# Optimization experiments

Measured on AMD Instinct MI355X. Metric: run time of the kernel, lower is better.

## Reference

```python
import jax, jax.numpy as jnp
import numpy as np


def setup_inputs() -> dict:
    key = jax.random.key(0)
    k1, k2 = jax.random.split(key)
    x = jax.random.normal(k1, (16, 512, 64, 64), dtype=jnp.float32)
    # learned scalar (nn.Parameter init zeros; use small random value so output is nontrivial)
    gamma = jax.random.normal(k2, (1,), dtype=jnp.float32) * 0.1
    return {"x": x, "gamma": gamma}


def reference(x, gamma):
    b, c, h, w = x.shape
    q = x.reshape(b, c, h * w)                      # [b, c, hw]
    energy = jnp.einsum('bcn,bdn->bcd', q, q)       # [b, c, c]
    # reverse-max trick: max - energy, then softmax over last dim
    energy_new = jnp.max(energy, axis=-1, keepdims=True) - energy
    attention = jax.nn.softmax(energy_new, axis=-1)  # [b, c, c]
    out = jnp.einsum('bcd,bdn->bcn', attention, q).reshape(b, c, h, w)
    return gamma * out + x
```

## Files before the change

### kernel.cpp

```cpp
#include <hip/hip_runtime.h>


constexpr int Bb = 16;
constexpr int Cc = 512;
constexpr int NN = 4096;

typedef _Float16 half8 __attribute__((ext_vector_type(8)));
typedef _Float16 half4 __attribute__((ext_vector_type(4)));
typedef float float4v __attribute__((ext_vector_type(4)));

__device__ inline void gld_lds16(const _Float16* g, _Float16* l) {
    __builtin_amdgcn_global_load_lds(
        (const __attribute__((address_space(1))) unsigned int*)g,
        (__attribute__((address_space(3))) unsigned int*)l, 16, 0, 0);
}

__global__ __launch_bounds__(256) void prep_kernel(const float* __restrict__ x,
                                                   _Float16* __restrict__ Qh,
                                                   _Float16* __restrict__ QhT) {
    __shared__ float T[64][65];
    const int b = blockIdx.z;
    const int n0 = blockIdx.x * 64;
    const int d0 = blockIdx.y * 64;
    const float* xb = x + ((size_t)b * Cc + d0) * NN + n0;
    const int tid = threadIdx.x;
#pragma unroll
    for (int i = 0; i < 4; ++i) {
        int lin = tid + i * 256;
        int dr = lin >> 4;
        int c4 = (lin & 15) * 4;
        float4 v = *reinterpret_cast<const float4*>(&xb[(size_t)dr * NN + c4]);
        T[dr][c4 + 0] = v.x; T[dr][c4 + 1] = v.y;
        T[dr][c4 + 2] = v.z; T[dr][c4 + 3] = v.w;
    }
    __syncthreads();
#pragma unroll
    for (int i = 0; i < 2; ++i) {
        int widx = tid + i * 256;
        int dr = widx >> 3;
        int cn = widx & 7;
        half8 h;
#pragma unroll
        for (int j = 0; j < 8; ++j) h[j] = (_Float16)T[dr][cn * 8 + j];
        size_t dst = ((size_t)b * Cc + d0 + dr) * NN + n0 + cn * 8;
        *reinterpret_cast<half8*>(&Qh[dst]) = h;
    }
#pragma unroll
    for (int i = 0; i < 2; ++i) {
        int widx = tid + i * 256;
        int nr = widx >> 3;
        int cd = widx & 7;
        half8 h;
#pragma unroll
        for (int j = 0; j < 8; ++j) h[j] = (_Float16)T[cd * 8 + j][nr];
        size_t dst = ((size_t)b * NN + n0 + nr) * Cc + d0 + cd * 8;
        *reinterpret_cast<half8*>(&QhT[dst]) = h;
    }
}

template <int NT, int SPLIT>
__global__ __launch_bounds__(512, 4) void gram_sym(const _Float16* __restrict__ A,
                                                   float* __restrict__ D) {
    __shared__ __align__(16) float gL[128 * 129];
    _Float16* sAB = (_Float16*)gL;
    const int BPB = 10 * SPLIT;
    const int L = blockIdx.x;
    const int t0 = (L & 7) * ((BPB * Bb) >> 3) + (L >> 3);
    const int b = t0 / BPB;
    const int rem = t0 % BPB;
    const int ti = rem / SPLIT;
    const int half = rem % SPLIT;
    const int kBase = half * NT * 64;
    float* Deff = D + (size_t)half * Bb * Cc * Cc;
    int tr, tc;
    if (ti < 4)      { tr = 0; tc = ti; }
    else if (ti < 7) { tr = 1; tc = ti - 3; }
    else if (ti < 9) { tr = 2; tc = ti - 5; }
    else             { tr = 3; tc = 3; }
    const int rowTile = tr * 128;
    const int colTile = tc * 128;

    const _Float16* Ab = A + (size_t)b * Cc * NN;
    const int tid = threadIdx.x;

    float4v acc[4][2];
#pragma unroll
    for (int m = 0; m < 4; ++m)
#pragma unroll
        for (int n = 0; n < 2; ++n) acc[m][n] = (float4v){0.f, 0.f, 0.f, 0.f};

    auto stage = [&](int buf, int kt) {
        const int k0 = kBase + (kt << 6);
        _Float16* sA = sAB + buf * 8192;
        _Float16* sB = sAB + 16384 + buf * 8192;
#pragma unroll
        for (int i = 0; i < 2; ++i) {
            int idx = tid + i * 512;
            int r = idx >> 3;
            int c = idx & 7;
            int cs = (c ^ (r & 7)) << 3;
            gld_lds16(Ab + (size_t)(rowTile + r) * NN + k0 + cs, sA + idx * 8);
            gld_lds16(Ab + (size_t)(colTile + r) * NN + k0 + cs, sB + idx * 8);
        }
    };

    stage(0, 0);
    __syncthreads();

    const int wid = tid >> 6, lane = tid & 63;
    const int wr = wid >> 2, wc = wid & 3;
    const int lr = lane & 15, q = lane >> 4;

    for (int t = 0; t < NT; ++t) {
        if (t + 1 < NT) stage((t + 1) & 1, t + 1);
        const _Float16* cA = sAB + (t & 1) * 8192;
        const _Float16* cB = sAB + 16384 + (t & 1) * 8192;
#pragma unroll
        for (int s = 0; s < 2; ++s) {
            half8 af[4], bf[2];
#pragma unroll
            for (int m = 0; m < 4; ++m) {
                int r = wr * 64 + m * 16 + lr;
                int c = (s * 4 + q) ^ (r & 7);
                af[m] = *reinterpret_cast<const half8*>(&cA[r * 64 + c * 8]);
            }
#pragma unroll
            for (int n = 0; n < 2; ++n) {
                int r = wc * 32 + n * 16 + lr;
                int c = (s * 4 + q) ^ (r & 7);
                bf[n] = *reinterpret_cast<const half8*>(&cB[r * 64 + c * 8]);
            }
#pragma unroll
            for (int m = 0; m < 4; ++m)
#pragma unroll
                for (int n = 0; n < 2; ++n)
                    acc[m][n] = __builtin_amdgcn_mfma_f32_16x16x32_f16(af[m], bf[n], acc[m][n], 0, 0, 0);
        }
        __syncthreads();
    }

    __syncthreads();
#pragma unroll
    for (int m = 0; m < 4; ++m)
#pragma unroll
        for (int n = 0; n < 2; ++n)
#pragma unroll
            for (int e = 0; e < 4; ++e)
                gL[(wr * 64 + m * 16 + q * 4 + e) * 129 + wc * 32 + n * 16 + lr] = acc[m][n][e];
    __syncthreads();

    float* Db = Deff + (size_t)b * Cc * Cc;
#pragma unroll
    for (int k = 0; k < 8; ++k) {
        int c = tid + k * 512;
        int row = c >> 5;
        int col = (c & 31) << 2;
        float4 v = *reinterpret_cast<const float4*>(&gL[row * 129 + col]);
        *reinterpret_cast<float4*>(&Db[(size_t)(rowTile + row) * Cc + colTile + col]) = v;
    }
    if (tr != tc) {
#pragma unroll
        for (int k = 0; k < 8; ++k) {
            int c = tid + k * 512;
            int crow = c >> 5;
            int r4 = (c & 31) << 2;
            float4 v;
            v.x = gL[(r4 + 0) * 129 + crow];
            v.y = gL[(r4 + 1) * 129 + crow];
            v.z = gL[(r4 + 2) * 129 + crow];
            v.w = gL[(r4 + 3) * 129 + crow];
            *reinterpret_cast<float4*>(&Db[(size_t)(colTile + crow) * Cc + rowTile + r4]) = v;
        }
    }
}

template <int RES>
__global__ __launch_bounds__(512, 6) void pv_mfma(const _Float16* __restrict__ A,
                                                  const _Float16* __restrict__ Bp,
                                                  const float* __restrict__ xres,
                                                  const _Float16* __restrict__ Qh,
                                                  const float* __restrict__ gamma,
                                                  float* __restrict__ out) {
    __shared__ __align__(16) _Float16 smem[5 * 4096];
    float* L = (float*)smem;
    const int BPB = 128;
    const int Lb = blockIdx.x;
    const int t0 = (Lb & 7) * ((BPB * Bb) >> 3) + (Lb >> 3);
    const int b = t0 / BPB;
    const int rem = t0 % BPB;
    const int rowTile = (rem & 3) * 128;
    const int colTile = (rem >> 2) * 128;

    const _Float16* Ab = A + (size_t)b * Cc * Cc;
    const _Float16* Bbp = Bp + (size_t)b * NN * Cc;
    const int tid = threadIdx.x;

    float4v acc[4][2];
#pragma unroll
    for (int m = 0; m < 4; ++m)
#pragma unroll
        for (int n = 0; n < 2; ++n) acc[m][n] = (float4v){0.f, 0.f, 0.f, 0.f};

    auto stageA = [&](_Float16* dst, int kt) {
        const int k0 = kt << 5;
        int r = tid >> 2, c = tid & 3;
        int cs = (c ^ ((r >> 1) & 3)) << 3;
        gld_lds16(Ab + (size_t)(rowTile + r) * Cc + k0 + cs, dst + tid * 8);
    };
    auto stageB = [&](_Float16* dst, int kt) {
        const int k0 = kt << 5;
        int r = tid >> 2, c = tid & 3;
        int cs = (c ^ ((r >> 1) & 3)) << 3;
        gld_lds16(Bbp + (size_t)(colTile + r) * Cc + k0 + cs, dst + tid * 8);
    };

    _Float16* sA0 = smem;
    _Float16* sA1 = smem + 4096;
    _Float16* sB_ = smem + 8192;

    stageA(sA0, 0);
    stageB(sB_, 0);
    stageB(sB_ + 4096, 1);

    const int wid = tid >> 6, lane = tid & 63;
    const int wr = wid >> 2, wc = wid & 3;
    const int lr = lane & 15, q = lane >> 4;

#pragma unroll
    for (int t = 0; t < 16; ++t) {
        if (t < 15) asm volatile("s_waitcnt vmcnt(1)" ::: "memory");
        else        asm volatile("s_waitcnt vmcnt(0)" ::: "memory");
        __builtin_amdgcn_s_barrier();
        __builtin_amdgcn_sched_barrier(0);

        const _Float16* cA = (t & 1) ? sA1 : sA0;
        const _Float16* cB = sB_ + (t % 3) * 4096;
        half8 af[4], bf[2];
#pragma unroll
        for (int m = 0; m < 4; ++m) {
            int r = wr * 64 + m * 16 + lr;
            int c = q ^ ((r >> 1) & 3);
            af[m] = *reinterpret_cast<const half8*>(&cA[r * 32 + c * 8]);
        }
#pragma unroll
        for (int n = 0; n < 2; ++n) {
            int r = wc * 32 + n * 16 + lr;
            int c = q ^ ((r >> 1) & 3);
            bf[n] = *reinterpret_cast<const half8*>(&cB[r * 32 + c * 8]);
        }
        if (t + 1 < 16) stageA((t & 1) ? sA0 : sA1, t + 1);
        if (t + 2 < 16) stageB(sB_ + ((t + 2) % 3) * 4096, t + 2);

        __builtin_amdgcn_s_setprio(1);
#pragma unroll
        for (int m = 0; m < 4; ++m)
#pragma unroll
            for (int n = 0; n < 2; ++n)
                acc[m][n] = __builtin_amdgcn_mfma_f32_16x16x32_f16(af[m], bf[n], acc[m][n], 0, 0, 0);
        __builtin_amdgcn_s_setprio(0);
    }

    const float g = gamma[0];
    const size_t base = (size_t)b * Cc * NN;
#pragma unroll
    for (int h = 0; h < 2; ++h) {
        __syncthreads();
        if (wr == h) {
#pragma unroll
            for (int m = 0; m < 4; ++m)
#pragma unroll
                for (int n = 0; n < 2; ++n)
#pragma unroll
                    for (int e = 0; e < 4; ++e)
                        L[(m * 16 + q * 4 + e) * 132 + wc * 32 + n * 16 + lr] = acc[m][n][e];
        }
        __syncthreads();
#pragma unroll
        for (int k = 0; k < 4; ++k) {
            int c2 = tid + k * 512;
            int row = c2 >> 5;
            int col = (c2 & 31) << 2;
            float4 v = *reinterpret_cast<const float4*>(&L[row * 132 + col]);
            size_t o = base + (size_t)(rowTile + h * 64 + row) * NN + colTile + col;
            float4 ov;
            if (RES == 0) {
                float4 xi = *reinterpret_cast<const float4*>(&xres[o]);
                ov.x = fmaf(g, v.x, xi.x); ov.y = fmaf(g, v.y, xi.y);
                ov.z = fmaf(g, v.z, xi.z); ov.w = fmaf(g, v.w, xi.w);
            } else {
                half4 hq = *reinterpret_cast<const half4*>(&Qh[o]);
                ov.x = fmaf(g, v.x, (float)hq[0]); ov.y = fmaf(g, v.y, (float)hq[1]);
                ov.z = fmaf(g, v.z, (float)hq[2]); ov.w = fmaf(g, v.w, (float)hq[3]);
            }
            *reinterpret_cast<float4*>(&out[o]) = ov;
        }
    }
}

template <int HALVES>
__global__ __launch_bounds__(256) void softmax_fp16(const float* __restrict__ eA,
                                                    const float* __restrict__ eB,
                                                    _Float16* __restrict__ attH) {
    const int wave = threadIdx.x >> 6;
    const int lane = threadIdx.x & 63;
    const int row = blockIdx.x * 4 + wave;
    const float* E1 = eA + (size_t)row * Cc;
    float v[8];
    {
        float4 a = *reinterpret_cast<const float4*>(&E1[lane * 8]);
        float4 c = *reinterpret_cast<const float4*>(&E1[lane * 8 + 4]);
        v[0] = a.x; v[1] = a.y; v[2] = a.z; v[3] = a.w;
        v[4] = c.x; v[5] = c.y; v[6] = c.z; v[7] = c.w;
    }
    if (HALVES == 2) {
        const float* E2 = eB + (size_t)row * Cc;
        float4 a = *reinterpret_cast<const float4*>(&E2[lane * 8]);
        float4 c = *reinterpret_cast<const float4*>(&E2[lane * 8 + 4]);
        v[0] += a.x; v[1] += a.y; v[2] += a.z; v[3] += a.w;
        v[4] += c.x; v[5] += c.y; v[6] += c.z; v[7] += c.w;
    }
    float mn = v[0];
#pragma unroll
    for (int i = 1; i < 8; ++i) mn = fminf(mn, v[i]);
#pragma unroll
    for (int off = 32; off; off >>= 1) mn = fminf(mn, __shfl_xor(mn, off, 64));
    float sum = 0.f;
#pragma unroll
    for (int i = 0; i < 8; ++i) {
        v[i] = __expf(mn - v[i]);
        sum += v[i];
    }
#pragma unroll
    for (int off = 32; off; off >>= 1) sum += __shfl_xor(sum, off, 64);
    const float inv = 1.0f / sum;
    half8 h;
#pragma unroll
    for (int i = 0; i < 8; ++i) h[i] = (_Float16)(v[i] * inv);
    *reinterpret_cast<half8*>(&attH[(size_t)row * Cc + lane * 8]) = h;
}

#define TILE 64
#define KT 32
#define PAD 68

__global__ __launch_bounds__(256) void gram_f32(const float* __restrict__ x,
                                                float* __restrict__ energy) {
    __shared__ __align__(16) float As[KT][PAD];
    __shared__ __align__(16) float Bs[KT][PAD];
    const int b = blockIdx.z;
    const int rowTile = blockIdx.y * TILE;
    const int colTile = blockIdx.x * TILE;
    const float* Q = x + (size_t)b * Cc * NN;
    const int t = threadIdx.x;
    const int tx = t & 15;
    const int ty = t >> 4;
    float acc[4][4] = {};
    for (int k0 = 0; k0 < NN; k0 += KT) {
#pragma unroll
        for (int i = 0; i < 8; ++i) {
            int idx = t + i * 256;
            int r = idx >> 5;
            int k = idx & 31;
            As[k][r] = Q[(size_t)(rowTile + r) * NN + k0 + k];
            Bs[k][r] = Q[(size_t)(colTile + r) * NN + k0 + k];
        }
        __syncthreads();
#pragma unroll
        for (int k = 0; k < KT; ++k) {
            float4 a = *reinterpret_cast<const float4*>(&As[k][ty * 4]);
            float4 bq = *reinterpret_cast<const float4*>(&Bs[k][tx * 4]);
            float av[4] = {a.x, a.y, a.z, a.w};
            float bv[4] = {bq.x, bq.y, bq.z, bq.w};
#pragma unroll
            for (int i = 0; i < 4; ++i)
#pragma unroll
                for (int j = 0; j < 4; ++j)
                    acc[i][j] = fmaf(av[i], bv[j], acc[i][j]);
        }
        __syncthreads();
    }
    float* E = energy + (size_t)b * Cc * Cc;
#pragma unroll
    for (int i = 0; i < 4; ++i) {
        const int rowG = rowTile + ty * 4 + i;
        float4 o;
        o.x = acc[i][0]; o.y = acc[i][1]; o.z = acc[i][2]; o.w = acc[i][3];
        *reinterpret_cast<float4*>(&E[(size_t)rowG * Cc + colTile + tx * 4]) = o;
    }
}

__global__ __launch_bounds__(256) void softmax_f32(float* __restrict__ energy) {
    const int wave = threadIdx.x >> 6;
    const int lane = threadIdx.x & 63;
    const int row = blockIdx.x * 4 + wave;
    float* E = energy + (size_t)row * Cc;
    float v[8];
    float mn = 3.4e38f;
#pragma unroll
    for (int i = 0; i < 8; ++i) {
        v[i] = E[lane + 64 * i];
        mn = fminf(mn, v[i]);
    }
#pragma unroll
    for (int off = 32; off; off >>= 1) mn = fminf(mn, __shfl_xor(mn, off, 64));
    float sum = 0.f;
#pragma unroll
    for (int i = 0; i < 8; ++i) {
        v[i] = __expf(mn - v[i]);
        sum += v[i];
    }
#pragma unroll
    for (int off = 32; off; off >>= 1) sum += __shfl_xor(sum, off, 64);
    const float inv = 1.0f / sum;
#pragma unroll
    for (int i = 0; i < 8; ++i) E[lane + 64 * i] = v[i] * inv;
}

__global__ __launch_bounds__(256) void pv_f32(const float* __restrict__ x,
                                              const float* __restrict__ att,
                                              const float* __restrict__ gamma,
                                              float* __restrict__ out) {
    __shared__ __align__(16) float As[KT][PAD];
    __shared__ __align__(16) float Bs[KT][PAD];
    const int b = blockIdx.z;
    const int rowTile = blockIdx.y * TILE;
    const int colTile = blockIdx.x * TILE;
    const float* Q = x + (size_t)b * Cc * NN;
    const float* A = att + (size_t)b * Cc * Cc;
    const int t = threadIdx.x;
    const int tx = t & 15;
    const int ty = t >> 4;
    float acc[4][4] = {};
    for (int k0 = 0; k0 < Cc; k0 += KT) {
#pragma unroll
        for (int i = 0; i < 8; ++i) {
            int idx = t + i * 256;
            {
                int r = idx >> 5, k = idx & 31;
                As[k][r] = A[(size_t)(rowTile + r) * Cc + k0 + k];
            }
            {
                int k = idx >> 6, c = idx & 63;
                Bs[k][c] = Q[(size_t)(k0 + k) * NN + colTile + c];
            }
        }
        __syncthreads();
#pragma unroll
        for (int k = 0; k < KT; ++k) {
            float4 a = *reinterpret_cast<const float4*>(&As[k][ty * 4]);
            float4 bq = *reinterpret_cast<const float4*>(&Bs[k][tx * 4]);
            float av[4] = {a.x, a.y, a.z, a.w};
            float bv[4] = {bq.x, bq.y, bq.z, bq.w};
#pragma unroll
            for (int i = 0; i < 4; ++i)
#pragma unroll
                for (int j = 0; j < 4; ++j)
                    acc[i][j] = fmaf(av[i], bv[j], acc[i][j]);
        }
        __syncthreads();
    }
    const float g = gamma[0];
#pragma unroll
    for (int i = 0; i < 4; ++i) {
        const int rowG = rowTile + ty * 4 + i;
        const size_t base = (size_t)rowG * NN + colTile + tx * 4;
        const float4 xi = *reinterpret_cast<const float4*>(&Q[base]);
        float4 o;
        o.x = fmaf(g, acc[i][0], xi.x);
        o.y = fmaf(g, acc[i][1], xi.y);
        o.z = fmaf(g, acc[i][2], xi.z);
        o.w = fmaf(g, acc[i][3], xi.w);
        *reinterpret_cast<float4*>(&out[(size_t)b * Cc * NN + base]) = o;
    }
}

extern "C" void kernel_launch(void* const* d_in, const int* in_sizes, int n_in,
                              void* d_out, int out_size, void* d_ws, size_t ws_size,
                              hipStream_t stream) {
    const float* x = (const float*)d_in[0];
    const float* gamma = (const float*)d_in[1];
    float* out = (float*)d_out;

    const size_t NQ = (size_t)Bb * Cc * NN;
    const size_t NE = (size_t)Bb * Cc * Cc;
    const size_t NEED1 = NQ * 2 * 2 + NE * 4 + NE * 2;
    const size_t NEED2 = NQ * 2 * 2 + NE * 4 * 2;
    const size_t NEED3 = NQ * 2 * 2 + NE * 4 * 2 + NE * 2;

    if (ws_size >= NEED3) {
        _Float16* Qh = (_Float16*)d_ws;
        _Float16* QhT = Qh + NQ;
        float* eA = (float*)(QhT + NQ);
        _Float16* attH = (_Float16*)(eA + 2 * NE);

        prep_kernel<<<dim3(NN / 64, Cc / 64, Bb), 256, 0, stream>>>(x, Qh, QhT);
        gram_sym<32, 2><<<dim3(20 * Bb), 512, 0, stream>>>(Qh, eA);
        softmax_fp16<2><<<dim3(Bb * Cc / 4), 256, 0, stream>>>(eA, eA + NE, attH);
        pv_mfma<1><<<dim3(128 * Bb), 512, 0, stream>>>(attH, QhT, x, Qh, gamma, out);
    } else if (ws_size >= NEED2) {
        _Float16* Qh = (_Float16*)d_ws;
        _Float16* QhT = Qh + NQ;
        float* eA = (float*)(QhT + NQ);
        _Float16* attH = Qh;

        prep_kernel<<<dim3(NN / 64, Cc / 64, Bb), 256, 0, stream>>>(x, Qh, QhT);
        gram_sym<32, 2><<<dim3(20 * Bb), 512, 0, stream>>>(Qh, eA);
        softmax_fp16<2><<<dim3(Bb * Cc / 4), 256, 0, stream>>>(eA, eA + NE, attH);
        pv_mfma<0><<<dim3(128 * Bb), 512, 0, stream>>>(attH, QhT, x, nullptr, gamma, out);
    } else if (ws_size >= NEED1) {
        _Float16* Qh = (_Float16*)d_ws;
        _Float16* QhT = Qh + NQ;
        float* energy = (float*)(QhT + NQ);
        _Float16* attH = (_Float16*)(energy + NE);

        prep_kernel<<<dim3(NN / 64, Cc / 64, Bb), 256, 0, stream>>>(x, Qh, QhT);
        gram_sym<64, 1><<<dim3(10 * Bb), 512, 0, stream>>>(Qh, energy);
        softmax_fp16<1><<<dim3(Bb * Cc / 4), 256, 0, stream>>>(energy, nullptr, attH);
        pv_mfma<1><<<dim3(128 * Bb), 512, 0, stream>>>(attH, QhT, x, Qh, gamma, out);
    } else {
        float* energy = (float*)d_ws;
        gram_f32<<<dim3(Cc / TILE, Cc / TILE, Bb), 256, 0, stream>>>(x, energy);
        softmax_f32<<<dim3(Bb * Cc / 4), 256, 0, stream>>>(energy);
        pv_f32<<<dim3(NN / TILE, Cc / TILE, Bb), 256, 0, stream>>>(x, energy, gamma, out);
    }
}
```

Baseline: 166.3 us.

## Switch attention-times-value GEMM to FP8 operands with fp8 MFMA

The attention matrix and the transposed input copy are stored as FP8 (e4m3 via cvt_pk_fp8) instead of FP16, and the PV GEMM uses the 16x16x32 fp8 MFMA with 64-byte K tiles, which halves operand bytes and LDS traffic. The workspace branches are consolidated, and the residual now always comes from the FP16 copy of x. The aim is to cut memory traffic and raise matrix throughput in the dominant PV stage. The cost is precision: softmax probabilities and x values quantised to FP8 lose accuracy, which could break tolerance.

```diff
diff --git a/kernel.cpp b/kernel.cpp
--- a/kernel.cpp
+++ b/kernel.cpp
@@ -14,10 +14,23 @@
         (const __attribute__((address_space(1))) unsigned int*)g,
         (__attribute__((address_space(3))) unsigned int*)l, 16, 0, 0);
 }
+__device__ inline void gld_lds16b(const unsigned char* g, unsigned char* l) {
+    __builtin_amdgcn_global_load_lds(
+        (const __attribute__((address_space(1))) unsigned int*)g,
+        (__attribute__((address_space(3))) unsigned int*)l, 16, 0, 0);
+}
+
+__device__ inline int2 pk_fp8x8(const float* v) {
+    int lo = __builtin_amdgcn_cvt_pk_fp8_f32(v[0], v[1], 0, false);
+    lo = __builtin_amdgcn_cvt_pk_fp8_f32(v[2], v[3], lo, true);
+    int hi = __builtin_amdgcn_cvt_pk_fp8_f32(v[4], v[5], 0, false);
+    hi = __builtin_amdgcn_cvt_pk_fp8_f32(v[6], v[7], hi, true);
+    return int2{lo, hi};
+}
 
 __global__ __launch_bounds__(256) void prep_kernel(const float* __restrict__ x,
                                                    _Float16* __restrict__ Qh,
-                                                   _Float16* __restrict__ QhT) {
+                                                   unsigned char* __restrict__ QhT8) {
     __shared__ float T[64][65];
     const int b = blockIdx.z;
     const int n0 = blockIdx.x * 64;
@@ -50,11 +63,12 @@
         int widx = tid + i * 256;
         int nr = widx >> 3;
         int cd = widx & 7;
-        half8 h;
-#pragma unroll
-        for (int j = 0; j < 8; ++j) h[j] = (_Float16)T[cd * 8 + j][nr];
+        float v[8];
+#pragma unroll
+        for (int j = 0; j < 8; ++j) v[j] = T[cd * 8 + j][nr];
+        int2 pk = pk_fp8x8(v);
         size_t dst = ((size_t)b * NN + n0 + nr) * Cc + d0 + cd * 8;
-        *reinterpret_cast<half8*>(&QhT[dst]) = h;
+        *reinterpret_cast<int2*>(&QhT8[dst]) = pk;
     }
 }
 
@@ -174,14 +188,12 @@
     }
 }
 
-template <int RES>
-__global__ __launch_bounds__(512, 6) void pv_mfma(const _Float16* __restrict__ A,
-                                                  const _Float16* __restrict__ Bp,
-                                                  const float* __restrict__ xres,
-                                                  const _Float16* __restrict__ Qh,
-                                                  const float* __restrict__ gamma,
-                                                  float* __restrict__ out) {
-    __shared__ __align__(16) _Float16 smem[5 * 4096];
+__global__ __launch_bounds__(512, 6) void pv_fp8(const unsigned char* __restrict__ A8,
+                                                 const unsigned char* __restrict__ B8,
+                                                 const _Float16* __restrict__ Qh,
+                                                 const float* __restrict__ gamma,
+                                                 float* __restrict__ out) {
+    __shared__ __align__(16) unsigned char smem[5 * 8192];
     float* L = (float*)smem;
     const int BPB = 128;
     const int Lb = blockIdx.x;
@@ -191,8 +203,8 @@
     const int rowTile = (rem & 3) * 128;
     const int colTile = (rem >> 2) * 128;
 
-    const _Float16* Ab = A + (size_t)b * Cc * Cc;
-    const _Float16* Bbp = Bp + (size_t)b * NN * Cc;
+    const unsigned char* Ab = A8 + (size_t)b * Cc * Cc;
+    const unsigned char* Bbp = B8 + (size_t)b * NN * Cc;
     const int tid = threadIdx.x;
 
     float4v acc[4][2];
@@ -201,62 +213,70 @@
 #pragma unroll
         for (int n = 0; n < 2; ++n) acc[m][n] = (float4v){0.f, 0.f, 0.f, 0.f};
 
-    auto stageA = [&](_Float16* dst, int kt) {
-        const int k0 = kt << 5;
+    auto stageA = [&](unsigned char* dst, int kt) {
+        const int k0 = kt << 6;
         int r = tid >> 2, c = tid & 3;
-        int cs = (c ^ ((r >> 1) & 3)) << 3;
-        gld_lds16(Ab + (size_t)(rowTile + r) * Cc + k0 + cs, dst + tid * 8);
+        int cs = (c ^ ((r >> 1) & 3)) << 4;
+        gld_lds16b(Ab + (size_t)(rowTile + r) * Cc + k0 + cs, dst + tid * 16);
     };
-    auto stageB = [&](_Float16* dst, int kt) {
-        const int k0 = kt << 5;
+    auto stageB = [&](unsigned char* dst, int kt) {
+        const int k0 = kt << 6;
         int r = tid >> 2, c = tid & 3;
-        int cs = (c ^ ((r >> 1) & 3)) << 3;
-        gld_lds16(Bbp + (size_t)(colTile + r) * Cc + k0 + cs, dst + tid * 8);
+        int cs = (c ^ ((r >> 1) & 3)) << 4;
+        gld_lds16b(Bbp + (size_t)(colTile + r) * Cc + k0 + cs, dst + tid * 16);
     };
 
-    _Float16* sA0 = smem;
-    _Float16* sA1 = smem + 4096;
-    _Float16* sB_ = smem + 8192;
+    unsigned char* sA0 = smem;
+    unsigned char* sA1 = smem + 8192;
+    unsigned char* sB_ = smem + 16384;
 
     stageA(sA0, 0);
     stageB(sB_, 0);
-    stageB(sB_ + 4096, 1);
+    stageB(sB_ + 8192, 1);
 
     const int wid = tid >> 6, lane = tid & 63;
     const int wr = wid >> 2, wc = wid & 3;
     const int lr = lane & 15, q = lane >> 4;
 
 #pragma unroll
-    for (int t = 0; t < 16; ++t) {
-        if (t < 15) asm volatile("s_waitcnt vmcnt(1)" ::: "memory");
-        else        asm volatile("s_waitcnt vmcnt(0)" ::: "memory");
+    for (int t = 0; t < 8; ++t) {
+        if (t < 7) asm volatile("s_waitcnt vmcnt(1)" ::: "memory");
+        else       asm volatile("s_waitcnt vmcnt(0)" ::: "memory");
         __builtin_amdgcn_s_barrier();
         __builtin_amdgcn_sched_barrier(0);
 
-        const _Float16* cA = (t & 1) ? sA1 : sA0;
-        const _Float16* cB = sB_ + (t % 3) * 4096;
-        half8 af[4], bf[2];
-#pragma unroll
-        for (int m = 0; m < 4; ++m) {
-            int r = wr * 64 + m * 16 + lr;
-            int c = q ^ ((r >> 1) & 3);
-            af[m] = *reinterpret_cast<const half8*>(&cA[r * 32 + c * 8]);
-        }
-#pragma unroll
-        for (int n = 0; n < 2; ++n) {
-            int r = wc * 32 + n * 16 + lr;
-            int c = q ^ ((r >> 1) & 3);
-            bf[n] = *reinterpret_cast<const half8*>(&cB[r * 32 + c * 8]);
-        }
-        if (t + 1 < 16) stageA((t & 1) ? sA0 : sA1, t + 1);
-        if (t + 2 < 16) stageB(sB_ + ((t + 2) % 3) * 4096, t + 2);
+        const unsigned char* cA = (t & 1) ? sA1 : sA0;
+        const unsigned char* cB = sB_ + (t % 3) * 8192;
+        long af[2][4];
+        long bf[2][2];
+#pragma unroll
+        for (int s = 0; s < 2; ++s) {
+            const int f = s * 4 + q;
+#pragma unroll
+            for (int m = 0; m < 4; ++m) {
+                int r = wr * 64 + m * 16 + lr;
+                int byt = r * 64 + (((f >> 1) ^ ((r >> 1) & 3)) << 4) + ((f & 1) << 3);
+                af[s][m] = *reinterpret_cast<const long*>(&cA[byt]);
+            }
+#pragma unroll
+            for (int n = 0; n < 2; ++n) {
+                int r = wc * 32 + n * 16 + lr;
+                int byt = r * 64 + (((f >> 1) ^ ((r >> 1) & 3)) << 4) + ((f & 1) << 3);
+                bf[s][n] = *reinterpret_cast<const long*>(&cB[byt]);
+            }
+        }
+        if (t + 1 < 8) stageA((t & 1) ? sA0 : sA1, t + 1);
+        if (t + 2 < 8) stageB(sB_ + ((t + 2) % 3) * 8192, t + 2);
 
         __builtin_amdgcn_s_setprio(1);
 #pragma unroll
-        for (int m = 0; m < 4; ++m)
-#pragma unroll
-            for (int n = 0; n < 2; ++n)
-                acc[m][n] = __builtin_amdgcn_mfma_f32_16x16x32_f16(af[m], bf[n], acc[m][n], 0, 0, 0);
+        for (int s = 0; s < 2; ++s)
+#pragma unroll
+            for (int m = 0; m < 4; ++m)
+#pragma unroll
+                for (int n = 0; n < 2; ++n)
+                    acc[m][n] = __builtin_amdgcn_mfma_f32_16x16x32_fp8_fp8(
+                        af[s][m], bf[s][n], acc[m][n], 0, 0, 0);
         __builtin_amdgcn_s_setprio(0);
     }
 
@@ -282,25 +302,19 @@
             int col = (c2 & 31) << 2;
             float4 v = *reinterpret_cast<const float4*>(&L[row * 132 + col]);
             size_t o = base + (size_t)(rowTile + h * 64 + row) * NN + colTile + col;
+            half4 hq = *reinterpret_cast<const half4*>(&Qh[o]);
             float4 ov;
-            if (RES == 0) {
-                float4 xi = *reinterpret_cast<const float4*>(&xres[o]);
-                ov.x = fmaf(g, v.x, xi.x); ov.y = fmaf(g, v.y, xi.y);
-                ov.z = fmaf(g, v.z, xi.z); ov.w = fmaf(g, v.w, xi.w);
-            } else {
-                half4 hq = *reinterpret_cast<const half4*>(&Qh[o]);
-                ov.x = fmaf(g, v.x, (float)hq[0]); ov.y = fmaf(g, v.y, (float)hq[1]);
-                ov.z = fmaf(g, v.z, (float)hq[2]); ov.w = fmaf(g, v.w, (float)hq[3]);
-            }
+            ov.x = fmaf(g, v.x, (float)hq[0]); ov.y = fmaf(g, v.y, (float)hq[1]);
+            ov.z = fmaf(g, v.z, (float)hq[2]); ov.w = fmaf(g, v.w, (float)hq[3]);
             *reinterpret_cast<float4*>(&out[o]) = ov;
         }
     }
 }
 
 template <int HALVES>
-__global__ __launch_bounds__(256) void softmax_fp16(const float* __restrict__ eA,
-                                                    const float* __restrict__ eB,
-                                                    _Float16* __restrict__ attH) {
+__global__ __launch_bounds__(256) void softmax_fp8(const float* __restrict__ eA,
+                                                   const float* __restrict__ eB,
+                                                   unsigned char* __restrict__ att8) {
     const int wave = threadIdx.x >> 6;
     const int lane = threadIdx.x & 63;
     const int row = blockIdx.x * 4 + wave;
@@ -333,10 +347,10 @@
 #pragma unroll
     for (int off = 32; off; off >>= 1) sum += __shfl_xor(sum, off, 64);
     const float inv = 1.0f / sum;
-    half8 h;
-#pragma unroll
-    for (int i = 0; i < 8; ++i) h[i] = (_Float16)(v[i] * inv);
-    *reinterpret_cast<half8*>(&attH[(size_t)row * Cc + lane * 8]) = h;
+#pragma unroll
+    for (int i = 0; i < 8; ++i) v[i] *= inv;
+    int2 pk = pk_fp8x8(v);
+    *reinterpret_cast<int2*>(&att8[(size_t)row * Cc + lane * 8]) = pk;
 }
 
 #define TILE 64
@@ -483,40 +497,26 @@
 
     const size_t NQ = (size_t)Bb * Cc * NN;
     const size_t NE = (size_t)Bb * Cc * Cc;
-    const size_t NEED1 = NQ * 2 * 2 + NE * 4 + NE * 2;
-    const size_t NEED2 = NQ * 2 * 2 + NE * 4 * 2;
-    const size_t NEED3 = NQ * 2 * 2 + NE * 4 * 2 + NE * 2;
-
-    if (ws_size >= NEED3) {
+    const size_t NEED2 = 2 * NQ + NQ + 8 * NE + NE;
+    const size_t NEED1 = 2 * NQ + NQ + 4 * NE + NE;
+
+    if (ws_size >= NEED1) {
         _Float16* Qh = (_Float16*)d_ws;
-        _Float16* QhT = Qh + NQ;
-        float* eA = (float*)(QhT + NQ);
-        _Float16* attH = (_Float16*)(eA + 2 * NE);
-
-        prep_kernel<<<dim3(NN / 64, Cc / 64, Bb), 256, 0, stream>>>(x, Qh, QhT);
-        gram_sym<32, 2><<<dim3(20 * Bb), 512, 0, stream>>>(Qh, eA);
-        softmax_fp16<2><<<dim3(Bb * Cc / 4), 256, 0, stream>>>(eA, eA + NE, attH);
-        pv_mfma<1><<<dim3(128 * Bb), 512, 0, stream>>>(attH, QhT, x, Qh, gamma, out);
-    } else if (ws_size >= NEED2) {
-        _Float16* Qh = (_Float16*)d_ws;
-        _Float16* QhT = Qh + NQ;
-        float* eA = (float*)(QhT + NQ);
-        _Float16* attH = Qh;
-
-        prep_kernel<<<dim3(NN / 64, Cc / 64, Bb), 256, 0, stream>>>(x, Qh, QhT);
-        gram_sym<32, 2><<<dim3(20 * Bb), 512, 0, stream>>>(Qh, eA);
-        softmax_fp16<2><<<dim3(Bb * Cc / 4), 256, 0, stream>>>(eA, eA + NE, attH);
-        pv_mfma<0><<<dim3(128 * Bb), 512, 0, stream>>>(attH, QhT, x, nullptr, gamma, out);
-    } else if (ws_size >= NEED1) {
-        _Float16* Qh = (_Float16*)d_ws;
-        _Float16* QhT = Qh + NQ;
-        float* energy = (float*)(QhT + NQ);
-        _Float16* attH = (_Float16*)(energy + NE);
-
-        prep_kernel<<<dim3(NN / 64, Cc / 64, Bb), 256, 0, stream>>>(x, Qh, QhT);
-        gram_sym<64, 1><<<dim3(10 * Bb), 512, 0, stream>>>(Qh, energy);
-        softmax_fp16<1><<<dim3(Bb * Cc / 4), 256, 0, stream>>>(energy, nullptr, attH);
-        pv_mfma<1><<<dim3(128 * Bb), 512, 0, stream>>>(attH, QhT, x, Qh, gamma, out);
+        unsigned char* QhT8 = (unsigned char*)(Qh + NQ);
+        float* eA = (float*)(QhT8 + NQ);
+
+        prep_kernel<<<dim3(NN / 64, Cc / 64, Bb), 256, 0, stream>>>(x, Qh, QhT8);
+        if (ws_size >= NEED2) {
+            unsigned char* att8 = (unsigned char*)(eA + 2 * NE);
+            gram_sym<32, 2><<<dim3(20 * Bb), 512, 0, stream>>>(Qh, eA);
+            softmax_fp8<2><<<dim3(Bb * Cc / 4), 256, 0, stream>>>(eA, eA + NE, att8);
+            pv_fp8<<<dim3(128 * Bb), 512, 0, stream>>>(att8, QhT8, Qh, gamma, out);
+        } else {
+            unsigned char* att8 = (unsigned char*)(eA + NE);
+            gram_sym<64, 1><<<dim3(10 * Bb), 512, 0, stream>>>(Qh, eA);
+            softmax_fp8<1><<<dim3(Bb * Cc / 4), 256, 0, stream>>>(eA, nullptr, att8);
+            pv_fp8<<<dim3(128 * Bb), 512, 0, stream>>>(att8, QhT8, Qh, gamma, out);
+        }
     } else {
         float* energy = (float*)d_ws;
         gram_f32<<<dim3(Cc / TILE, Cc / TILE, Bb), 256, 0, stream>>>(x, energy);
```

Result: faster. 138.4 us (-16.8%).
